# Kernel tuning notes

Measured on AMD Instinct MI355X. Metric: run time of the kernel, lower is better.

The kernel has to match this reference:

```python
import jax, jax.numpy as jnp
import numpy as np

T, B, H, I = 128, 32, 256, 256


def setup_inputs() -> dict:
    key = jax.random.key(0)
    ks = jax.random.split(key, 8)
    s = 0.05
    embs = jax.random.normal(ks[0], (T, B, I), jnp.float32)
    lens = jax.random.randint(ks[1], (B,), 1, T + 1)  # lengths in [1, T]
    W_ih = jax.random.normal(ks[2], (4 * H, I), jnp.float32) * s
    W_hh = jax.random.normal(ks[3], (4 * H, H), jnp.float32) * s
    b_ih = jax.random.normal(ks[4], (4 * H,), jnp.float32) * s
    b_hh = jax.random.normal(ks[5], (4 * H,), jnp.float32) * s
    W_a = jax.random.normal(ks[6], (H, 2 * H), jnp.float32) * s  # attention combine (Luong-style)
    b_a = jax.random.normal(ks[7], (H,), jnp.float32) * s
    return {"embs": embs, "lens": lens, "W_ih": W_ih, "W_hh": W_hh,
            "b_ih": b_ih, "b_hh": b_hh, "W_a": W_a, "b_a": b_a}


def reference(embs, lens, W_ih, W_hh, b_ih, b_hh, W_a, b_a):
    Tn, Bn, _ = embs.shape
    Hn = W_hh.shape[1]
    t_idx = jnp.arange(Tn)

    def step(carry, inp):
        h, c, buf, h_fin, c_fin = carry  # h,c: [B,H]; buf: [T,B,H] history of outputs
        t, emb = inp
        # dot-product attention of current hidden over past outputs (steps < t)
        scores = jnp.einsum('tbh,bh->tb', buf, h)
        valid = (t_idx < t)[:, None]
        alpha = jax.nn.softmax(jnp.where(valid, scores, -1e9), axis=0)
        ctx = jnp.einsum('tb,tbh->bh', alpha, buf)
        h_att = jnp.tanh(jnp.concatenate([ctx, h], axis=-1) @ W_a.T + b_a)
        h = jnp.where(t > 0, h_att, h)  # no history at t=0
        # standard PyTorch LSTM cell (gate order i,f,g,o)
        gates = emb @ W_ih.T + b_ih + h @ W_hh.T + b_hh
        i_g, f_g, g_g, o_g = jnp.split(gates, 4, axis=-1)
        c = jax.nn.sigmoid(f_g) * c + jax.nn.sigmoid(i_g) * jnp.tanh(g_g)
        h = jax.nn.sigmoid(o_g) * jnp.tanh(c)
        buf = buf.at[t].set(h)
        take = (t == lens - 1)[:, None]
        h_fin = jnp.where(take, h, h_fin)
        c_fin = jnp.where(take, c, c_fin)
        return (h, c, buf, h_fin, c_fin), h

    z = jnp.zeros((Bn, Hn), embs.dtype)
    buf0 = jnp.zeros((Tn, Bn, Hn), embs.dtype)
    carry, output = jax.lax.scan(step, (z, z, buf0, z, z), (t_idx, embs))
    # output: [T,B,H]; final (h,c) gathered at t == lens-1: [B,H]
    return output, carry[3], carry[4]
```

## Files before the change

kernel.cpp:

```cpp
#include <hip/hip_runtime.h>


#define T_DIM 128
#define B_DIM 32

typedef _Float16 half2_t __attribute__((ext_vector_type(2)));

static __device__ __forceinline__ unsigned pack2(float a, float b) {
  half2_t h;
  h.x = (_Float16)a;
  h.y = (_Float16)b;
  return __builtin_bit_cast(unsigned, h);
}

static __device__ __forceinline__ float dot2f(unsigned w, unsigned v, float acc) {
  half2_t a = __builtin_bit_cast(half2_t, w);
  half2_t b = __builtin_bit_cast(half2_t, v);
#if __has_builtin(__builtin_amdgcn_fdot2)
  return __builtin_amdgcn_fdot2(a, b, acc, false);
#else
  return acc + (float)a.x * (float)b.x + (float)a.y * (float)b.y;
#endif
}

static __device__ __forceinline__ float dot8(uint4 w, uint4 v, float acc) {
  acc = dot2f(w.x, v.x, acc);
  acc = dot2f(w.y, v.y, acc);
  acc = dot2f(w.z, v.z, acc);
  acc = dot2f(w.w, v.w, acc);
  return acc;
}

static __device__ __forceinline__ float lo16(unsigned u) {
  return (float)__builtin_bit_cast(half2_t, u).x;
}
static __device__ __forceinline__ float hi16(unsigned u) {
  return (float)__builtin_bit_cast(half2_t, u).y;
}

static __device__ __forceinline__ float fsig(float x) {
  return __builtin_amdgcn_rcpf(1.f + __expf(-x));
}
static __device__ __forceinline__ float ftanh(float x) {
  float e = __expf(2.f * x);
  return 1.f - 2.f * __builtin_amdgcn_rcpf(e + 1.f);
}

__global__ void pack_weights(const float* __restrict__ W_ih, const float* __restrict__ W_hh,
                             const float* __restrict__ W_a, float* __restrict__ W_ihT,
                             uint4* __restrict__ Whh_pack, uint4* __restrict__ Wa_pack,
                             unsigned long long* __restrict__ ywp,
                             unsigned long long* __restrict__ psx) {
  int n = blockIdx.x * 256 + threadIdx.x;
  {
    int k = n >> 10, r = n & 1023;
    W_ihT[n] = W_ih[r * 256 + k];
  }
  if (n < 32768) {
    int m = n >> 12, tid = (n >> 3) & 511, i = n & 7;
    int r_local = tid >> 2, qk = tid & 3;
    int q = r_local >> 5, jl = r_local & 31;
    int r = q * 256 + m * 32 + jl;
    const float* src = W_hh + r * 256 + (4 * i + qk) * 8;
    uint4 v;
    v.x = pack2(src[0], src[1]);
    v.y = pack2(src[2], src[3]);
    v.z = pack2(src[4], src[5]);
    v.w = pack2(src[6], src[7]);
    Whh_pack[n] = v;
  }
  if (n < 16384) {
    int m = n >> 11, j = (n >> 3) & 255, c = n & 7;
    int col0 = (c < 4) ? (m * 32 + c * 8) : (256 + m * 32 + (c - 4) * 8);
    const float* src = W_a + j * 512 + col0;
    uint4 v;
    v.x = pack2(src[0], src[1]);
    v.y = pack2(src[2], src[3]);
    v.z = pack2(src[4], src[5]);
    v.w = pack2(src[6], src[7]);
    Wa_pack[n] = v;
  }
  if (n < 65536)
    __hip_atomic_store(&ywp[n], 0ull, __ATOMIC_RELAXED, __HIP_MEMORY_SCOPE_AGENT);
  else if (n < 81920)
    __hip_atomic_store(&psx[n - 65536], 0ull, __ATOMIC_RELAXED, __HIP_MEMORY_SCOPE_AGENT);
}

__global__ void compute_gih(const float* __restrict__ embs, const float* __restrict__ W_ihT,
                            const float* __restrict__ b_ih, const float* __restrict__ b_hh,
                            float* __restrict__ gih) {
  __shared__ float embS[8][256];
  const int tid = threadIdx.x;
  const int tb0 = blockIdx.x * 8;
#pragma unroll
  for (int e = 0; e < 8; ++e) embS[e][tid] = embs[(size_t)(tb0 + e) * 256 + tid];
  __syncthreads();
  float acc[8][4];
#pragma unroll
  for (int e = 0; e < 8; ++e)
#pragma unroll
    for (int q = 0; q < 4; ++q) acc[e][q] = 0.f;
  for (int k = 0; k < 256; ++k) {
    float w0 = W_ihT[k * 1024 + tid];
    float w1 = W_ihT[k * 1024 + tid + 256];
    float w2 = W_ihT[k * 1024 + tid + 512];
    float w3 = W_ihT[k * 1024 + tid + 768];
#pragma unroll
    for (int e = 0; e < 8; ++e) {
      float x = embS[e][k];
      acc[e][0] += x * w0;
      acc[e][1] += x * w1;
      acc[e][2] += x * w2;
      acc[e][3] += x * w3;
    }
  }
#pragma unroll
  for (int q = 0; q < 4; ++q) {
    float bias = b_ih[q * 256 + tid] + b_hh[q * 256 + tid];
#pragma unroll
    for (int e = 0; e < 8; ++e)
      gih[(size_t)(tb0 + e) * 1024 + q * 256 + tid] = acc[e][q] + bias;
  }
}

__global__ void __launch_bounds__(512, 1)
alstm_rec(const int* __restrict__ lens, const float* __restrict__ gih,
          const uint4* __restrict__ Whh_pack, const uint4* __restrict__ Wa_pack,
          const float* __restrict__ b_a, unsigned long long* __restrict__ ywp,
          unsigned long long* __restrict__ psx, float* __restrict__ out,
          float* __restrict__ hfin, float* __restrict__ cfin) {
  const int tid = threadIdx.x;
  const int b = blockIdx.x & 31;
  const int m = blockIdx.x >> 5;

  __shared__ __align__(16) unsigned histSl[128 * 18];
  __shared__ __align__(16) float ystoreF[128 * 256];
  __shared__ __align__(16) unsigned hp2[128];
  __shared__ __align__(16) unsigned hsl2[16];
  __shared__ float sc[128];
  __shared__ float zp[4][256];
  __shared__ float gsl[128];

  uint4 wh4[8];
  {
    const uint4* p = Whh_pack + ((size_t)m * 512 + tid) * 8;
#pragma unroll
    for (int i = 0; i < 8; ++i) wh4[i] = p[i];
  }
  uint4 way[4], waw[4];
  {
    const int j_pub = (tid - 128) & 255;
    const uint4* p = Wa_pack + ((size_t)m * 256 + j_pub) * 8;
#pragma unroll
    for (int i = 0; i < 4; ++i) way[i] = p[i];
#pragma unroll
    for (int i = 0; i < 4; ++i) waw[i] = p[4 + i];
  }
  const float ba_j = (tid < 256) ? b_a[tid] : 0.f;
  const int len_b = lens[b];
  const int r_local = tid >> 2, qk = tid & 3;
  const int gq = r_local >> 5, gjl = r_local & 31;

  if (tid < 128) hp2[tid] = 0u;
  float c_reg = 0.f;
  __syncthreads();

  for (int t = 0; t < T_DIM; ++t) {
    float gih_v = gih[((size_t)t * 32 + b) * 1024 + gq * 256 + m * 32 + gjl];
    float w_j = 0.f;

    if (t > 0) {
      if (tid < 256) {
        const unsigned long long* base = ywp + b * 2048 + tid;
        unsigned long long v[8];
        for (;;) {
          bool ok = true;
#pragma unroll
          for (int mm = 0; mm < 8; ++mm)
            v[mm] = __hip_atomic_load(base + mm * 256, __ATOMIC_RELAXED, __HIP_MEMORY_SCOPE_AGENT);
#pragma unroll
          for (int mm = 0; mm < 8; ++mm) ok &= ((unsigned)v[mm] == (unsigned)t);
          if (ok) break;
          __builtin_amdgcn_s_sleep(1);
        }
        float y = 0.f, w = 0.f;
#pragma unroll
        for (int mm = 0; mm < 8; ++mm) {
          unsigned pl = (unsigned)(v[mm] >> 32);
          y += lo16(pl);
          w += hi16(pl);
        }
        w_j = w;
        ystoreF[(t - 1) * 256 + tid] = y;
      } else if (tid < 320) {
        const int p = tid - 256;
        const unsigned long long* base = psx + b * 512 + p;
        unsigned long long v[8];
        for (;;) {
          bool ok = true;
#pragma unroll
          for (int mm = 0; mm < 8; ++mm)
            v[mm] = __hip_atomic_load(base + mm * 64, __ATOMIC_RELAXED, __HIP_MEMORY_SCOPE_AGENT);
#pragma unroll
          for (int mm = 0; mm < 8; ++mm) ok &= ((unsigned)v[mm] == (unsigned)t);
          if (ok) break;
          __builtin_amdgcn_s_sleep(1);
        }
        float s0 = 0.f, s1 = 0.f;
#pragma unroll
        for (int mm = 0; mm < 8; ++mm) {
          unsigned pl = (unsigned)(v[mm] >> 32);
          s0 += lo16(pl);
          s1 += hi16(pl);
        }
        sc[2 * p] = s0;
        sc[2 * p + 1] = s1;
      }
      __syncthreads();
      if (tid < 64) {
        float v0 = (tid < t) ? sc[tid] : -3.0e38f;
        float v1 = (tid + 64 < t) ? sc[tid + 64] : -3.0e38f;
        float mx = fmaxf(v0, v1);
#pragma unroll
        for (int off = 32; off >= 1; off >>= 1) mx = fmaxf(mx, __shfl_xor(mx, off));
        float e0 = (tid < t) ? __expf(v0 - mx) : 0.f;
        float e1 = (tid + 64 < t) ? __expf(v1 - mx) : 0.f;
        float sm = e0 + e1;
#pragma unroll
        for (int off = 32; off >= 1; off >>= 1) sm += __shfl_xor(sm, off);
        float inv = __builtin_amdgcn_rcpf(sm);
        sc[tid] = e0 * inv;
        sc[tid + 64] = e1 * inv;
      }
      __syncthreads();
      {
        const int sp = tid >> 7, p2 = tid & 127;
        float c0 = 0.f, c1 = 0.f;
        const float* yb = ystoreF + 2 * p2;
        for (int s = sp; s < t; s += 4) {
          float al = sc[s];
          float2 yv = *(const float2*)(yb + s * 256);
          c0 += al * yv.x;
          c1 += al * yv.y;
        }
        zp[sp][2 * p2] = c0;
        zp[sp][2 * p2 + 1] = c1;
      }
      __syncthreads();
      if (tid < 256) {
        float z = zp[0][tid] + zp[1][tid] + zp[2][tid] + zp[3][tid];
        float hv = ftanh(ba_j + w_j + z);
        float o = __shfl_xor(hv, 1);
        if (!(tid & 1)) hp2[tid >> 1] = pack2(hv, o);
      }
      __syncthreads();
    }
    {
      float a = 0.f;
#pragma unroll
      for (int i = 0; i < 8; ++i) {
        const int c = 4 * i + qk;
        uint4 hv = *(const uint4*)&hp2[c << 2];
        a = dot8(wh4[i], hv, a);
      }
      a += __shfl_xor(a, 1);
      a += __shfl_xor(a, 2);
      if (qk == 0) gsl[r_local] = a + gih_v;
    }
    __syncthreads();
    if (tid < 32) {
      float ig = fsig(gsl[tid]);
      float fg = fsig(gsl[32 + tid]);
      float gg = ftanh(gsl[64 + tid]);
      float og = fsig(gsl[96 + tid]);
      float cn = fg * c_reg + ig * gg;
      float hn = og * ftanh(cn);
      c_reg = cn;
      out[((size_t)t * 32 + b) * 256 + m * 32 + tid] = hn;
      if (t == len_b - 1) {
        hfin[b * 256 + m * 32 + tid] = hn;
        cfin[b * 256 + m * 32 + tid] = cn;
      }
      float o = __shfl_xor(hn, 1);
      if (!(tid & 1)) {
        unsigned u = pack2(hn, o);
        hsl2[tid >> 1] = u;
        histSl[t * 18 + (tid >> 1)] = u;
      }
    }
    __syncthreads();
    if (tid < 128) {
      float a = 0.f;
#pragma unroll
      for (int k = 0; k < 8; ++k) {
        uint2 hw = *(const uint2*)&histSl[tid * 18 + 2 * k];
        uint2 qv = *(const uint2*)&hsl2[2 * k];
        a = dot2f(hw.x, qv.x, a);
        a = dot2f(hw.y, qv.y, a);
      }
      float o = __shfl_xor(a, 1);
      if (!(tid & 1)) {
        unsigned long long v = ((unsigned long long)pack2(a, o) << 32) |
                               (unsigned long long)(unsigned)(t + 1);
        __hip_atomic_store(&psx[b * 512 + m * 64 + (tid >> 1)], v, __ATOMIC_RELAXED,
                           __HIP_MEMORY_SCOPE_AGENT);
      }
    } else if (tid < 384) {
      const int j = tid - 128;
      float ay = 0.f, aw = 0.f;
#pragma unroll
      for (int c = 0; c < 4; ++c) {
        uint4 hv = *(const uint4*)&hsl2[c * 4];
        ay = dot8(way[c], hv, ay);
        aw = dot8(waw[c], hv, aw);
      }
      unsigned long long v = ((unsigned long long)pack2(ay, aw) << 32) |
                             (unsigned long long)(unsigned)(t + 1);
      __hip_atomic_store(&ywp[b * 2048 + m * 256 + j], v, __ATOMIC_RELAXED,
                         __HIP_MEMORY_SCOPE_AGENT);
    }
  }
}

extern "C" void kernel_launch(void* const* d_in, const int* in_sizes, int n_in,
                              void* d_out, int out_size, void* d_ws, size_t ws_size,
                              hipStream_t stream) {
  const float* embs = (const float*)d_in[0];
  const int* lens = (const int*)d_in[1];
  const float* W_ih = (const float*)d_in[2];
  const float* W_hh = (const float*)d_in[3];
  const float* b_ih = (const float*)d_in[4];
  const float* b_hh = (const float*)d_in[5];
  const float* W_a = (const float*)d_in[6];
  const float* b_a = (const float*)d_in[7];

  float* out = (float*)d_out;
  float* hfin = out + (size_t)T_DIM * B_DIM * 256;
  float* cfin = hfin + (size_t)B_DIM * 256;

  char* ws = (char*)d_ws;
  float* gih = (float*)ws;
  float* W_ihT = (float*)(ws + 16777216);
  uint4* Whh_pack = (uint4*)(ws + 17825792);
  uint4* Wa_pack = (uint4*)(ws + 18350080);
  unsigned long long* ywp = (unsigned long long*)(ws + 18612224);
  unsigned long long* psx = (unsigned long long*)(ws + 19136512);

  pack_weights<<<1024, 256, 0, stream>>>(W_ih, W_hh, W_a, W_ihT, Whh_pack, Wa_pack, ywp, psx);
  compute_gih<<<512, 256, 0, stream>>>(embs, W_ihT, b_ih, b_hh, gih);
  alstm_rec<<<256, 512, 0, stream>>>(lens, gih, Whh_pack, Wa_pack, b_a, ywp, psx, out, hfin,
                                     cfin);
}
```

Baseline: 563.2 us.

## Remove per-step barriers by computing LSTM cell redundantly in every wavefront

```diff
diff --git a/kernel.cpp b/kernel.cpp
--- a/kernel.cpp
+++ b/kernel.cpp
@@ -136,9 +136,8 @@
   __shared__ __align__(16) unsigned histSl[128 * 18];
   __shared__ __align__(16) float ystoreF[128 * 256];
   __shared__ __align__(16) unsigned hp2[128];
-  __shared__ __align__(16) unsigned hsl2[16];
-  __shared__ float sc[128];
-  __shared__ float zp[4][256];
+  __shared__ __align__(16) float sc[128];
+  __shared__ __align__(16) float zp[8][256];
   __shared__ float gsl[128];
 
   uint4 wh4[8];
@@ -213,42 +212,45 @@
           s0 += lo16(pl);
           s1 += hi16(pl);
         }
-        sc[2 * p] = s0;
-        sc[2 * p + 1] = s1;
-      }
-      __syncthreads();
-      if (tid < 64) {
-        float v0 = (tid < t) ? sc[tid] : -3.0e38f;
-        float v1 = (tid + 64 < t) ? sc[tid + 64] : -3.0e38f;
+        float v0 = (2 * p < t) ? s0 : -3.0e38f;
+        float v1 = (2 * p + 1 < t) ? s1 : -3.0e38f;
         float mx = fmaxf(v0, v1);
 #pragma unroll
         for (int off = 32; off >= 1; off >>= 1) mx = fmaxf(mx, __shfl_xor(mx, off));
-        float e0 = (tid < t) ? __expf(v0 - mx) : 0.f;
-        float e1 = (tid + 64 < t) ? __expf(v1 - mx) : 0.f;
+        float e0 = (2 * p < t) ? __expf(v0 - mx) : 0.f;
+        float e1 = (2 * p + 1 < t) ? __expf(v1 - mx) : 0.f;
         float sm = e0 + e1;
 #pragma unroll
         for (int off = 32; off >= 1; off >>= 1) sm += __shfl_xor(sm, off);
         float inv = __builtin_amdgcn_rcpf(sm);
-        sc[tid] = e0 * inv;
-        sc[tid + 64] = e1 * inv;
+        sc[2 * p] = e0 * inv;
+        sc[2 * p + 1] = e1 * inv;
       }
       __syncthreads();
       {
-        const int sp = tid >> 7, p2 = tid & 127;
-        float c0 = 0.f, c1 = 0.f;
-        const float* yb = ystoreF + 2 * p2;
-        for (int s = sp; s < t; s += 4) {
+        const int sp = tid >> 6, cg = tid & 63;
+        float c0 = 0.f, c1 = 0.f, c2 = 0.f, c3 = 0.f;
+        const float* yb = ystoreF + 4 * cg;
+        for (int s = sp; s < t; s += 8) {
           float al = sc[s];
-          float2 yv = *(const float2*)(yb + s * 256);
+          const float4 yv = *(const float4*)(yb + (size_t)s * 256);
           c0 += al * yv.x;
           c1 += al * yv.y;
-        }
-        zp[sp][2 * p2] = c0;
-        zp[sp][2 * p2 + 1] = c1;
+          c2 += al * yv.z;
+          c3 += al * yv.w;
+        }
+        float4 st;
+        st.x = c0;
+        st.y = c1;
+        st.z = c2;
+        st.w = c3;
+        *(float4*)&zp[sp][4 * cg] = st;
       }
       __syncthreads();
       if (tid < 256) {
-        float z = zp[0][tid] + zp[1][tid] + zp[2][tid] + zp[3][tid];
+        float z = 0.f;
+#pragma unroll
+        for (int p = 0; p < 8; ++p) z += zp[p][tid];
         float hv = ftanh(ba_j + w_j + z);
         float o = __shfl_xor(hv, 1);
         if (!(tid & 1)) hp2[tid >> 1] = pack2(hv, o);
@@ -256,67 +258,85 @@
       __syncthreads();
     }
     {
-      float a = 0.f;
-#pragma unroll
-      for (int i = 0; i < 8; ++i) {
-        const int c = 4 * i + qk;
-        uint4 hv = *(const uint4*)&hp2[c << 2];
-        a = dot8(wh4[i], hv, a);
-      }
+      float a0 = 0.f, a1 = 0.f;
+#pragma unroll
+      for (int i = 0; i < 8; i += 2) {
+        uint4 hv0 = *(const uint4*)&hp2[(4 * i + qk) << 2];
+        uint4 hv1 = *(const uint4*)&hp2[(4 * (i + 1) + qk) << 2];
+        a0 = dot8(wh4[i], hv0, a0);
+        a1 = dot8(wh4[i + 1], hv1, a1);
+      }
+      float a = a0 + a1;
       a += __shfl_xor(a, 1);
       a += __shfl_xor(a, 2);
       if (qk == 0) gsl[r_local] = a + gih_v;
     }
     __syncthreads();
-    if (tid < 32) {
-      float ig = fsig(gsl[tid]);
-      float fg = fsig(gsl[32 + tid]);
-      float gg = ftanh(gsl[64 + tid]);
-      float og = fsig(gsl[96 + tid]);
+    unsigned hq[16];
+    {
+      const int sl = tid & 31;
+      float ig = fsig(gsl[sl]);
+      float fg = fsig(gsl[32 + sl]);
+      float gg = ftanh(gsl[64 + sl]);
+      float og = fsig(gsl[96 + sl]);
       float cn = fg * c_reg + ig * gg;
       float hn = og * ftanh(cn);
       c_reg = cn;
-      out[((size_t)t * 32 + b) * 256 + m * 32 + tid] = hn;
-      if (t == len_b - 1) {
-        hfin[b * 256 + m * 32 + tid] = hn;
-        cfin[b * 256 + m * 32 + tid] = cn;
+      if (tid >= 384 && tid < 416) {
+        out[((size_t)t * 32 + b) * 256 + m * 32 + sl] = hn;
+        if (t == len_b - 1) {
+          hfin[b * 256 + m * 32 + sl] = hn;
+          cfin[b * 256 + m * 32 + sl] = cn;
+        }
       }
       float o = __shfl_xor(hn, 1);
-      if (!(tid & 1)) {
-        unsigned u = pack2(hn, o);
-        hsl2[tid >> 1] = u;
-        histSl[t * 18 + (tid >> 1)] = u;
-      }
-    }
-    __syncthreads();
+      unsigned u = pack2(hn, o);
+      if (tid >= 384 && tid < 416 && !(tid & 1)) histSl[t * 18 + (sl >> 1)] = u;
+#pragma unroll
+      for (int k = 0; k < 16; ++k) hq[k] = __shfl(u, 2 * k);
+    }
     if (tid < 128) {
-      float a = 0.f;
-#pragma unroll
-      for (int k = 0; k < 8; ++k) {
-        uint2 hw = *(const uint2*)&histSl[tid * 18 + 2 * k];
-        uint2 qv = *(const uint2*)&hsl2[2 * k];
-        a = dot2f(hw.x, qv.x, a);
-        a = dot2f(hw.y, qv.y, a);
-      }
+      float a0 = 0.f, a1 = 0.f;
+      if (tid == t) {
+#pragma unroll
+        for (int k = 0; k < 8; ++k) {
+          a0 = dot2f(hq[2 * k], hq[2 * k], a0);
+          a1 = dot2f(hq[2 * k + 1], hq[2 * k + 1], a1);
+        }
+      } else {
+#pragma unroll
+        for (int k = 0; k < 8; ++k) {
+          uint2 hw = *(const uint2*)&histSl[tid * 18 + 2 * k];
+          a0 = dot2f(hw.x, hq[2 * k], a0);
+          a1 = dot2f(hw.y, hq[2 * k + 1], a1);
+        }
+      }
+      float a = a0 + a1;
       float o = __shfl_xor(a, 1);
       if (!(tid & 1)) {
-        unsigned long long v = ((unsigned long long)pack2(a, o) << 32) |
-                               (unsigned long long)(unsigned)(t + 1);
-        __hip_atomic_store(&psx[b * 512 + m * 64 + (tid >> 1)], v, __ATOMIC_RELAXED,
+        unsigned long long vv = ((unsigned long long)pack2(a, o) << 32) |
+                                (unsigned long long)(unsigned)(t + 1);
+        __hip_atomic_store(&psx[b * 512 + m * 64 + (tid >> 1)], vv, __ATOMIC_RELAXED,
                            __HIP_MEMORY_SCOPE_AGENT);
       }
     } else if (tid < 384) {
       const int j = tid - 128;
-      float ay = 0.f, aw = 0.f;
-#pragma unroll
-      for (int c = 0; c < 4; ++c) {
-        uint4 hv = *(const uint4*)&hsl2[c * 4];
-        ay = dot8(way[c], hv, ay);
-        aw = dot8(waw[c], hv, aw);
-      }
-      unsigned long long v = ((unsigned long long)pack2(ay, aw) << 32) |
-                             (unsigned long long)(unsigned)(t + 1);
-      __hip_atomic_store(&ywp[b * 2048 + m * 256 + j], v, __ATOMIC_RELAXED,
+      uint4 hv0 = make_uint4(hq[0], hq[1], hq[2], hq[3]);
+      uint4 hv1 = make_uint4(hq[4], hq[5], hq[6], hq[7]);
+      uint4 hv2 = make_uint4(hq[8], hq[9], hq[10], hq[11]);
+      uint4 hv3 = make_uint4(hq[12], hq[13], hq[14], hq[15]);
+      float ay0 = 0.f, ay1 = 0.f, aw0 = 0.f, aw1 = 0.f;
+      ay0 = dot8(way[0], hv0, ay0);
+      aw0 = dot8(waw[0], hv0, aw0);
+      ay1 = dot8(way[1], hv1, ay1);
+      aw1 = dot8(waw[1], hv1, aw1);
+      ay0 = dot8(way[2], hv2, ay0);
+      aw0 = dot8(waw[2], hv2, aw0);
+      ay1 = dot8(way[3], hv3, ay1);
+      aw1 = dot8(waw[3], hv3, aw1);
+      unsigned long long vv = ((unsigned long long)pack2(ay0 + ay1, aw0 + aw1) << 32) |
+                              (unsigned long long)(unsigned)(t + 1);
+      __hip_atomic_store(&ywp[b * 2048 + m * 256 + j], vv, __ATOMIC_RELAXED,
                          __HIP_MEMORY_SCOPE_AGENT);
     }
   }
```

After: 539.0 us. 4.3% less time.
